# Kernel tuning notes

Measured on AMD Instinct MI355X. Metric: run time of the kernel, lower is better.

## Reference

```python
import jax, jax.numpy as jnp
import numpy as np

NEG = -1e30  # stand-in for -inf that keeps gradients finite


def setup_inputs() -> dict:
    key = jax.random.key(0)
    k0, k1, k2 = jax.random.split(key, 3)
    B, S, W, K = 48, 128, 4, 256
    logits = jax.random.normal(k0, (B, S, W, K), dtype=jnp.float32)
    T = jax.random.normal(k1, (B, K, K), dtype=jnp.float32)
    hamming_cost = jax.random.uniform(k2, (B, S, W, K), dtype=jnp.float32)
    tag_mask = jnp.ones((B, K, K), dtype=jnp.float32)
    text_mask = jnp.ones((B, S), dtype=jnp.int32)
    return dict(logits=logits, T=T, hamming_cost=hamming_cost,
                tag_mask=tag_mask, text_mask=text_mask)


def reference(logits, T, hamming_cost, tag_mask, text_mask):
    # Semi-Markov CRF partition function (use_transition_layer == 'True').
    B, S, W, K = logits.shape
    lg = jnp.transpose(logits, (1, 2, 0, 3))        # (S, W, B, K)
    hc = jnp.transpose(hamming_cost, (1, 2, 0, 3))  # (S, W, B, K)
    # emission score for a span of width w+1 ending at j, labeled k
    emit_all = (lg + hc) * tag_mask[:, 0, :]        # (S, W, B, K)
    tranT = T * tag_mask                            # (B, K, Kprev)
    w_idx = jnp.arange(W)

    # buf[w] = alpha[j - w]; rows with j - w < 0 held at NEG (excluded)
    buf0 = jnp.full((W, B, K), NEG, dtype=jnp.float32).at[0].set(0.0)

    def step(buf, inp):
        emit_j, j = inp  # emit_j: (W, B, K)
        # transition applies only when the previous alpha is a real segment
        # boundary (w < j); the w == j row connects to the initial state.
        tran = jnp.where((w_idx < j)[:, None, None, None], tranT[None], 0.0)
        # scores[w, b, k, kp] = alpha[j-w, b, kp] + T'[b, k, kp] + emit[w, b, k]
        scores = buf[:, :, None, :] + tran + emit_j[:, :, :, None]
        alpha_j = jax.nn.logsumexp(scores, axis=(0, 3))  # (B, K)
        buf = jnp.concatenate([alpha_j[None], buf[:-1]], axis=0)
        return buf, alpha_j

    _, alphas = jax.lax.scan(step, buf0, (emit_all, jnp.arange(S)))
    full = jnp.concatenate([jnp.zeros((1, B, K), dtype=jnp.float32), alphas], axis=0)
    ls = jax.nn.logsumexp(full, axis=-1)            # (S+1, B)
    lengths = jnp.sum(text_mask, axis=1)            # (B,)
    partition = ls[lengths, jnp.arange(B)]          # (B,)
    return partition[None]                          # (1, B) as in torch code
```

## Files before the change

### kernel.cpp

```cpp
#include <hip/hip_runtime.h>
#include <hip/hip_bf16.h>
#include <type_traits>

typedef __attribute__((ext_vector_type(8))) _Float16 half8;
typedef __attribute__((ext_vector_type(4))) _Float16 half4;
typedef __attribute__((ext_vector_type(2))) _Float16 half2;
typedef __attribute__((ext_vector_type(4))) float f32x4;

constexpr int CB = 48, CS = 128, CW = 4, CK = 256;
constexpr int LDP = 264;

__global__ void prep_eT_kernel(const f32x4* __restrict__ T,
                               const f32x4* __restrict__ tm,
                               half4* __restrict__ eT, int n4) {
    int i = blockIdx.x * 256 + threadIdx.x;
    if (i < n4) {
        f32x4 t = T[i], m = tm[i];
        half4 o;
        o[0] = (_Float16)__expf(t[0] * m[0]);
        o[1] = (_Float16)__expf(t[1] * m[1]);
        o[2] = (_Float16)__expf(t[2] * m[2]);
        o[3] = (_Float16)__expf(t[3] * m[3]);
        eT[i] = o;
    }
}

__global__ __launch_bounds__(256, 1)
void crf_scan_kernel(const float* __restrict__ logits,
                     const float* __restrict__ ham,
                     const _Float16* __restrict__ eT,
                     const float* __restrict__ tag_mask,
                     const int* __restrict__ text_mask,
                     float* __restrict__ out) {
    const int b = blockIdx.x;
    const int tid = (int)threadIdx.x;
    const int wv = tid >> 6;
    const int lane = tid & 63;
    const int l16 = lane & 15;
    const int g4 = lane >> 4;

    __shared__ alignas(16) _Float16 ebuf[16 * LDP];
    __shared__ alignas(16) float ylds[CK][4];
    __shared__ float red[4];
    __shared__ int len_s;

    for (int i = tid; i < 16 * LDP; i += 256) ebuf[i] = (_Float16)0.0f;
    if (tid == 0) len_s = 0;
    __syncthreads();
    ebuf[3 * LDP + tid] = (_Float16)1.0f;
    if (tid < CS) atomicAdd(&len_s, text_mask[b * CS + tid]);

    const float tm0 = tag_mask[(size_t)b * CK * CK + tid];

    half8 bfr[8][4];
    const _Float16* eTb = eT + (size_t)b * CK * CK;
#pragma unroll
    for (int c = 0; c < 8; ++c)
#pragma unroll
        for (int t = 0; t < 4; ++t) {
            int k = wv * 64 + t * 16 + l16;
            bfr[c][t] = *(const half8*)(eTb + (size_t)k * CK + c * 32 + g4 * 8);
        }

    const float* lgb = logits + (size_t)b * CS * CW * CK;
    const float* hcb = ham    + (size_t)b * CS * CW * CK;

    float mr[4] = {0.0f, 0.0f, 0.0f, 0.0f};
    float ls_prev = __logf(256.0f) - 2.0f;
    float out_r = __logf(256.0f);
    float e_last = 0.0f, M_last = 0.0f;

    float em_cur[4];
#pragma unroll
    for (int w = 0; w < 4; ++w)
        em_cur[w] = (lgb[w * CK + tid] + hcb[w * CK + tid]) * tm0;

    __syncthreads();
    const int len = len_s;

    const half2 one2 = {(_Float16)1.0f, (_Float16)1.0f};

    auto step = [&](int j, auto uc, auto firstc) {
        constexpr int u = uc.value;
        constexpr bool first = firstc.value;
        constexpr int sp = (u + 3) & 3;

        half8 af[8];
#pragma unroll
        for (int c = 0; c < 8; ++c)
            af[c] = *(const half8*)(ebuf + l16 * LDP + c * 32 + g4 * 8);

        int jn = (j + 1 < CS) ? j + 1 : 0;
        float lgn[4], hcn[4];
#pragma unroll
        for (int w = 0; w < 4; ++w) {
            int idx = jn * (CW * CK) + w * CK + tid;
            lgn[w] = lgb[idx];
            hcn[w] = hcb[idx];
        }

        float rs0 = 0.0f, rs1 = 0.0f;
#pragma unroll
        for (int c = 0; c < 8; ++c) {
#pragma unroll
            for (int p = 0; p < 4; p += 2) {
                half2 h0 = {af[c][2 * p], af[c][2 * p + 1]};
                half2 h1 = {af[c][2 * p + 2], af[c][2 * p + 3]};
                rs0 = __builtin_amdgcn_fdot2(h0, one2, rs0, false);
                rs1 = __builtin_amdgcn_fdot2(h1, one2, rs1, false);
            }
        }
        float rs = rs0 + rs1;
        rs += __shfl_xor(rs, 16, 64);
        rs += __shfl_xor(rs, 32, 64);
        float sum_prev = __shfl(rs, sp, 64);

        float lsj = mr[sp] + __logf(sum_prev);
        if (j == len) out_r = lsj;
        float delta = lsj - ls_prev;
        ls_prev = lsj;
        float Mj = lsj + delta;
        float C = mr[sp];

        f32x4 acc[4];
#pragma unroll
        for (int t = 0; t < 4; ++t) acc[t] = (f32x4){0.0f, 0.0f, 0.0f, 0.0f};
#pragma unroll
        for (int c = 0; c < 8; ++c)
#pragma unroll
            for (int t = 0; t < 4; ++t)
                acc[t] = __builtin_amdgcn_mfma_f32_16x16x32_f16(af[c], bfr[c][t], acc[t], 0, 0, 0);

        if (lane < 16) {
#pragma unroll
            for (int t = 0; t < 4; ++t)
                *(f32x4*)(&ylds[wv * 64 + t * 16 + l16][0]) = acc[t];
        }
        f32x4 y = *(const f32x4*)(&ylds[tid][0]);

        float S = 0.0f;
#pragma unroll
        for (int w = 0; w < 4; ++w) {
            const int sw = (u + 3 - w) & 3;
            float yv = y[sw];
            if (first) {
                if (w == j) yv = 256.0f;
                else if (w > j) yv = 0.0f;
            }
            S = fmaf(yv, __expf(mr[sw] + em_cur[w] - C), S);
        }
        float e = S * __expf(C - Mj);
        ebuf[u * LDP + tid] = (_Float16)e;
        e_last = e;
        M_last = Mj;
        mr[u] = Mj;

#pragma unroll
        for (int w = 0; w < 4; ++w)
            em_cur[w] = (lgn[w] + hcn[w]) * tm0;

        __syncthreads();
    };

#define IC(v) std::integral_constant<int, v>{}
#define BC(v) std::integral_constant<bool, v>{}
    step(0, IC(0), BC(true));
    step(1, IC(1), BC(true));
    step(2, IC(2), BC(true));
    step(3, IC(3), BC(true));
    for (int jj = 4; jj < CS; jj += 4) {
        step(jj + 0, IC(0), BC(false));
        step(jj + 1, IC(1), BC(false));
        step(jj + 2, IC(2), BC(false));
        step(jj + 3, IC(3), BC(false));
    }
#undef IC
#undef BC

    float s = e_last;
#pragma unroll
    for (int o = 32; o; o >>= 1) s += __shfl_xor(s, o, 64);
    if (lane == 0) red[wv] = s;
    __syncthreads();
    if (tid == 0) {
        float tot = red[0] + red[1] + red[2] + red[3];
        float ls_full = M_last + __logf(tot);
        if (len == CS) out_r = ls_full;
        out[b] = out_r;
    }
}

extern "C" void kernel_launch(void* const* d_in, const int* in_sizes, int n_in,
                              void* d_out, int out_size, void* d_ws, size_t ws_size,
                              hipStream_t stream) {
    const float* logits    = (const float*)d_in[0];
    const float* T         = (const float*)d_in[1];
    const float* ham       = (const float*)d_in[2];
    const float* tag_mask  = (const float*)d_in[3];
    const int*   text_mask = (const int*)d_in[4];
    float* out = (float*)d_out;

    _Float16* eT = (_Float16*)d_ws;
    int n4 = CB * CK * CK / 4;
    prep_eT_kernel<<<(n4 + 255) / 256, 256, 0, stream>>>(
        (const f32x4*)T, (const f32x4*)tag_mask, (half4*)eT, n4);
    crf_scan_kernel<<<CB, 256, 0, stream>>>(logits, ham, eT, tag_mask, text_mask, out);
}
```

Before: 198.7 us.

## Replace per-step MFMA over four lags with per-thread fdot2 on newest alpha

Before, every step ran MFMAs over a 16-row LDS buffer, recomputing the transition products for all four buffered alphas. Now each thread holds its own row of exp(T) in registers and, with fdot2 over a double-buffered LDS vector, computes the product only for the newest alpha; the three older products are carried forward in registers. The ylds round trip and the cross-lane row-sum shuffle are gone: a per-wave row sum is written to a double-buffered reduction array before one raw barrier per step. This removes redundant matrix work and LDS traffic on the serial critical path. In exchange it adds a 64-lane shuffle reduction per step and puts 128 VGPRs of eT in registers.

```diff
diff --git a/kernel.cpp b/kernel.cpp
--- a/kernel.cpp
+++ b/kernel.cpp
@@ -8,7 +8,6 @@
 typedef __attribute__((ext_vector_type(4))) float f32x4;
 
 constexpr int CB = 48, CS = 128, CW = 4, CK = 256;
-constexpr int LDP = 264;
 
 __global__ void prep_eT_kernel(const f32x4* __restrict__ T,
                                const f32x4* __restrict__ tm,
@@ -36,39 +35,34 @@
     const int tid = (int)threadIdx.x;
     const int wv = tid >> 6;
     const int lane = tid & 63;
-    const int l16 = lane & 15;
-    const int g4 = lane >> 4;
 
-    __shared__ alignas(16) _Float16 ebuf[16 * LDP];
-    __shared__ alignas(16) float ylds[CK][4];
-    __shared__ float red[4];
+    __shared__ alignas(16) _Float16 ebuf[2][CK];
+    __shared__ alignas(16) float red[2][4];
     __shared__ int len_s;
 
-    for (int i = tid; i < 16 * LDP; i += 256) ebuf[i] = (_Float16)0.0f;
+    ebuf[1][tid] = (_Float16)1.0f;
+    ebuf[0][tid] = (_Float16)0.0f;
+    if (tid < 4) { red[0][tid] = 0.0f; red[1][tid] = 64.0f; }
     if (tid == 0) len_s = 0;
     __syncthreads();
-    ebuf[3 * LDP + tid] = (_Float16)1.0f;
     if (tid < CS) atomicAdd(&len_s, text_mask[b * CS + tid]);
 
     const float tm0 = tag_mask[(size_t)b * CK * CK + tid];
 
-    half8 bfr[8][4];
-    const _Float16* eTb = eT + (size_t)b * CK * CK;
+    half8 etv[32];
+    {
+        const _Float16* rowp = eT + (size_t)b * CK * CK + (size_t)tid * CK;
 #pragma unroll
-    for (int c = 0; c < 8; ++c)
-#pragma unroll
-        for (int t = 0; t < 4; ++t) {
-            int k = wv * 64 + t * 16 + l16;
-            bfr[c][t] = *(const half8*)(eTb + (size_t)k * CK + c * 32 + g4 * 8);
-        }
+        for (int c = 0; c < 32; ++c) etv[c] = *(const half8*)(rowp + 8 * c);
+    }
 
     const float* lgb = logits + (size_t)b * CS * CW * CK;
     const float* hcb = ham    + (size_t)b * CS * CW * CK;
 
-    float mr[4] = {0.0f, 0.0f, 0.0f, 0.0f};
+    float Mn = 0.0f, M1 = 0.0f, M2 = 0.0f, M3 = 0.0f;
+    float y1 = 0.0f, y2 = 0.0f, y3 = 0.0f;
     float ls_prev = __logf(256.0f) - 2.0f;
     float out_r = __logf(256.0f);
-    float e_last = 0.0f, M_last = 0.0f;
 
     float em_cur[4];
 #pragma unroll
@@ -78,17 +72,11 @@
     __syncthreads();
     const int len = len_s;
 
-    const half2 one2 = {(_Float16)1.0f, (_Float16)1.0f};
+    auto step = [&](int j, auto prc) {
+        constexpr int PR = prc.value;
+        constexpr int PW = PR ^ 1;
 
-    auto step = [&](int j, auto uc, auto firstc) {
-        constexpr int u = uc.value;
-        constexpr bool first = firstc.value;
-        constexpr int sp = (u + 3) & 3;
-
-        half8 af[8];
-#pragma unroll
-        for (int c = 0; c < 8; ++c)
-            af[c] = *(const half8*)(ebuf + l16 * LDP + c * 32 + g4 * 8);
+        f32x4 redv = *(const f32x4*)(&red[PR][0]);
 
         int jn = (j + 1 < CS) ? j + 1 : 0;
         float lgn[4], hcn[4];
@@ -99,92 +87,83 @@
             hcn[w] = hcb[idx];
         }
 
-        float rs0 = 0.0f, rs1 = 0.0f;
+        float a0 = 0.0f, a1 = 0.0f, a2 = 0.0f, a3 = 0.0f;
 #pragma unroll
-        for (int c = 0; c < 8; ++c) {
+        for (int g = 0; g < 8; ++g) {
+            half8 ev[4];
 #pragma unroll
-            for (int p = 0; p < 4; p += 2) {
-                half2 h0 = {af[c][2 * p], af[c][2 * p + 1]};
-                half2 h1 = {af[c][2 * p + 2], af[c][2 * p + 3]};
-                rs0 = __builtin_amdgcn_fdot2(h0, one2, rs0, false);
-                rs1 = __builtin_amdgcn_fdot2(h1, one2, rs1, false);
+            for (int c = 0; c < 4; ++c)
+                ev[c] = *(const half8*)(&ebuf[PR][(g * 4 + c) * 8]);
+#pragma unroll
+            for (int c = 0; c < 4; ++c) {
+                const int ch = g * 4 + c;
+                half2 e0 = {ev[c][0], ev[c][1]}, t0 = {etv[ch][0], etv[ch][1]};
+                half2 e1 = {ev[c][2], ev[c][3]}, t1 = {etv[ch][2], etv[ch][3]};
+                half2 e2 = {ev[c][4], ev[c][5]}, t2 = {etv[ch][4], etv[ch][5]};
+                half2 e3 = {ev[c][6], ev[c][7]}, t3 = {etv[ch][6], etv[ch][7]};
+                a0 = __builtin_amdgcn_fdot2(e0, t0, a0, false);
+                a1 = __builtin_amdgcn_fdot2(e1, t1, a1, false);
+                a2 = __builtin_amdgcn_fdot2(e2, t2, a2, false);
+                a3 = __builtin_amdgcn_fdot2(e3, t3, a3, false);
             }
         }
-        float rs = rs0 + rs1;
-        rs += __shfl_xor(rs, 16, 64);
-        rs += __shfl_xor(rs, 32, 64);
-        float sum_prev = __shfl(rs, sp, 64);
+        float y_new = (a0 + a1) + (a2 + a3);
 
-        float lsj = mr[sp] + __logf(sum_prev);
+        float sum_prev = (redv[0] + redv[1]) + (redv[2] + redv[3]);
+        float lsj = Mn + __logf(sum_prev);
         if (j == len) out_r = lsj;
         float delta = lsj - ls_prev;
         ls_prev = lsj;
         float Mj = lsj + delta;
-        float C = mr[sp];
+        float C = Mn;
 
-        f32x4 acc[4];
-#pragma unroll
-        for (int t = 0; t < 4; ++t) acc[t] = (f32x4){0.0f, 0.0f, 0.0f, 0.0f};
-#pragma unroll
-        for (int c = 0; c < 8; ++c)
-#pragma unroll
-            for (int t = 0; t < 4; ++t)
-                acc[t] = __builtin_amdgcn_mfma_f32_16x16x32_f16(af[c], bfr[c][t], acc[t], 0, 0, 0);
-
-        if (lane < 16) {
-#pragma unroll
-            for (int t = 0; t < 4; ++t)
-                *(f32x4*)(&ylds[wv * 64 + t * 16 + l16][0]) = acc[t];
+        float S;
+        {
+            float yv = y_new;
+            if (j == 0) yv = 256.0f;
+            S = yv * __expf(Mn + em_cur[0] - C);
         }
-        f32x4 y = *(const f32x4*)(&ylds[tid][0]);
-
-        float S = 0.0f;
-#pragma unroll
-        for (int w = 0; w < 4; ++w) {
-            const int sw = (u + 3 - w) & 3;
-            float yv = y[sw];
-            if (first) {
-                if (w == j) yv = 256.0f;
-                else if (w > j) yv = 0.0f;
-            }
-            S = fmaf(yv, __expf(mr[sw] + em_cur[w] - C), S);
+        {
+            float yv = y1;
+            if (j < 4) yv = (j == 1) ? 256.0f : (j < 1 ? 0.0f : yv);
+            S = fmaf(yv, __expf(M1 + em_cur[1] - C), S);
+        }
+        {
+            float yv = y2;
+            if (j < 4) yv = (j == 2) ? 256.0f : (j < 2 ? 0.0f : yv);
+            S = fmaf(yv, __expf(M2 + em_cur[2] - C), S);
+        }
+        {
+            float yv = y3;
+            if (j < 4) yv = (j == 3) ? 256.0f : (j < 3 ? 0.0f : yv);
+            S = fmaf(yv, __expf(M3 + em_cur[3] - C), S);
         }
         float e = S * __expf(C - Mj);
-        ebuf[u * LDP + tid] = (_Float16)e;
-        e_last = e;
-        M_last = Mj;
-        mr[u] = Mj;
+        ebuf[PW][tid] = (_Float16)e;
+
+        float ps = e;
+#pragma unroll
+        for (int o = 1; o < 64; o <<= 1) ps += __shfl_xor(ps, o, 64);
+        if (lane == 0) red[PW][wv] = ps;
+
+        y3 = y2; y2 = y1; y1 = y_new;
+        M3 = M2; M2 = M1; M1 = Mn; Mn = Mj;
 
 #pragma unroll
         for (int w = 0; w < 4; ++w)
             em_cur[w] = (lgn[w] + hcn[w]) * tm0;
 
-        __syncthreads();
+        asm volatile("s_waitcnt expcnt(0) lgkmcnt(0)\n\ts_barrier" ::: "memory");
     };
 
-#define IC(v) std::integral_constant<int, v>{}
-#define BC(v) std::integral_constant<bool, v>{}
-    step(0, IC(0), BC(true));
-    step(1, IC(1), BC(true));
-    step(2, IC(2), BC(true));
-    step(3, IC(3), BC(true));
-    for (int jj = 4; jj < CS; jj += 4) {
-        step(jj + 0, IC(0), BC(false));
-        step(jj + 1, IC(1), BC(false));
-        step(jj + 2, IC(2), BC(false));
-        step(jj + 3, IC(3), BC(false));
+    for (int j = 0; j < CS; j += 2) {
+        step(j,     std::integral_constant<int, 1>{});
+        step(j + 1, std::integral_constant<int, 0>{});
     }
-#undef IC
-#undef BC
 
-    float s = e_last;
-#pragma unroll
-    for (int o = 32; o; o >>= 1) s += __shfl_xor(s, o, 64);
-    if (lane == 0) red[wv] = s;
-    __syncthreads();
     if (tid == 0) {
-        float tot = red[0] + red[1] + red[2] + red[3];
-        float ls_full = M_last + __logf(tot);
+        float tot = (red[1][0] + red[1][1]) + (red[1][2] + red[1][3]);
+        float ls_full = Mn + __logf(tot);
         if (len == CS) out_r = ls_full;
         out[b] = out_r;
     }
```

Result: slower. 236.1 us (+18.8%).
